# Kernel tuning notes

Measured on AMD Instinct MI355X. Metric: run time of the kernel, lower is better.

Reference implementation:

```python
import jax, jax.numpy as jnp
import numpy as np

B, S, T = 32, 256, 256
V, E, H, C, SE = 10000, 512, 1024, 1024, 8


def _gru_cell(x, h, Wih, Whh, bih, bhh):
    # torch.nn.GRUCell math; Wih: [3H, in], Whh: [3H, H]
    gi = x @ Wih.T + bih
    gh = h @ Whh.T + bhh
    ir, iz, inn = jnp.split(gi, 3, axis=-1)
    hr, hz, hn = jnp.split(gh, 3, axis=-1)
    r = jax.nn.sigmoid(ir + hr)
    z = jax.nn.sigmoid(iz + hz)
    n = jnp.tanh(inn + r * hn)
    return (1.0 - z) * n + z * h


def setup_inputs() -> dict:
    key = jax.random.key(0)
    ks = jax.random.split(key, 20)
    s = 0.02
    emb_table = jax.random.normal(ks[0], (V, E), jnp.float32) * s
    emb_table = emb_table.at[0].set(0.0)  # padding_idx = 0
    style_table = jax.random.normal(ks[1], (2, SE), jnp.float32)
    in1 = E + SE + C
    inp = {
        "enc_output": jax.random.normal(ks[2], (B, S, C), jnp.float32),
        "enc_len": jax.random.randint(ks[3], (B,), 1, S + 1),
        "styles": jax.random.randint(ks[4], (B,), 0, 2),
        "dec_in": jax.random.randint(ks[5], (B, T), 0, V),
        "dec_out": jax.random.randint(ks[6], (B, T), 0, V),
        "emb_table": emb_table,
        "style_table": style_table,
        "Wp": jax.random.normal(ks[7], (H, C + SE), jnp.float32) * s,
        "bp": jnp.zeros((H,), jnp.float32),
        "Wih1": jax.random.normal(ks[8], (3 * H, in1), jnp.float32) * s,
        "Whh1": jax.random.normal(ks[9], (3 * H, H), jnp.float32) * s,
        "bih1": jnp.zeros((3 * H,), jnp.float32),
        "bhh1": jnp.zeros((3 * H,), jnp.float32),
        "Wih2": jax.random.normal(ks[10], (3 * H, H), jnp.float32) * s,
        "Whh2": jax.random.normal(ks[11], (3 * H, H), jnp.float32) * s,
        "bih2": jnp.zeros((3 * H,), jnp.float32),
        "bhh2": jnp.zeros((3 * H,), jnp.float32),
        "Wout": jax.random.normal(ks[12], (H, V), jnp.float32) * s,
        "bout": jnp.zeros((V,), jnp.float32),
    }
    return inp


def reference(enc_output, enc_len, styles, dec_in, dec_out, emb_table, style_table,
              Wp, bp, Wih1, Whh1, bih1, bhh1, Wih2, Whh2, bih2, bhh2, Wout, bout):
    batch = enc_output.shape[0]
    # get_enc_context: encoder output at last valid timestep
    last = jnp.clip(enc_len - 1, 0, enc_output.shape[1] - 1)
    ctx = enc_output[jnp.arange(batch), last]              # [B, C]
    style_emb = style_table[styles]                         # [B, SE]
    # init hidden state: project(concat(ctx, style_emb))
    h0 = jnp.concatenate([ctx, style_emb], -1) @ Wp.T + bp  # [B, H]
    h1 = jnp.zeros_like(h0)
    # constant part of cell input (no attention: context fixed)
    sc = jnp.concatenate([style_emb, ctx], -1)              # [B, SE+C]
    emb_seq = emb_table[dec_in].transpose(1, 0, 2)          # [T, B, E]

    def step(carry, emb_t):
        a, b = carry
        x = jnp.concatenate([emb_t, sc], -1)
        a = _gru_cell(x, a, Wih1, Whh1, bih1, bhh1)
        b = _gru_cell(a, b, Wih2, Whh2, bih2, bhh2)
        return (a, b), b

    _, h1s = jax.lax.scan(step, (h0, h1), emb_seq)          # [T, B, H]
    logits = jnp.einsum('tbh,hv->btv', h1s, Wout) + bout    # [B, T, V]
    log_probs = jax.nn.log_softmax(logits, axis=2)
    prediction = jnp.argmax(logits, axis=-1)                # [B, T]
    dec_output_log_probs = jnp.take_along_axis(log_probs, dec_out[..., None], axis=2)[..., 0]
    return logits, dec_output_log_probs, prediction
```

## Files before the change

### kernel.cpp

```cpp
#include <hip/hip_runtime.h>
#include <math.h>

#define NBLK 256
#define GROUPS 16
#define GSIZE 16

__device__ __forceinline__ float sigf(float x) { return 1.0f / (1.0f + __expf(-x)); }

__global__ void prep_kernel(const float* __restrict__ enc_output,
                            const int*   __restrict__ enc_len,
                            const int*   __restrict__ styles,
                            const float* __restrict__ style_table,
                            float* __restrict__ xA,
                            float* __restrict__ xB,
                            float* __restrict__ bT0)
{
    int b = blockIdx.x;
    int tid = threadIdx.x;
    int last = enc_len[b] - 1;
    last = last < 0 ? 0 : (last > 255 ? 255 : last);
    const float* ctx = enc_output + ((size_t)b * 256 + last) * 1024;
    for (int k = tid; k < 1024; k += blockDim.x) {
        float v = ctx[k];
        xA[b * 1032 + k]     = v;
        xB[b * 1032 + 8 + k] = v;
        bT0[b * 1024 + k]    = 0.0f;
    }
    if (tid < 8) {
        float se = style_table[styles[b] * 8 + tid];
        xA[b * 1032 + 1024 + tid] = se;
        xB[b * 1032 + tid]        = se;
    }
}

template<int BMODE, int EPI, int GATHER>
__global__ __launch_bounds__(256, 2)
void gemm128(const float* __restrict__ A, int lda,
             const float* __restrict__ W, int ldb,
             const float* __restrict__ bias,
             const float* __restrict__ rowbase,
             const int*   __restrict__ gidx,
             float* __restrict__ Cout,
             int M, int N, int K)
{
    __shared__ float As[8][132];
    __shared__ float Bs[8][132];
    const int tid = threadIdx.x;
    const int r0 = blockIdx.x * 128;
    const int n0 = blockIdx.y * 128;
    const int tx = tid & 15;
    const int ty = tid >> 4;

    float acc[8][8];
#pragma unroll
    for (int i = 0; i < 8; ++i)
#pragma unroll
        for (int j = 0; j < 8; ++j) acc[i][j] = 0.0f;

    const int am  = tid >> 1;
    const int akq = (tid & 1) * 4;
    const bool avalid = (r0 + am) < M;
    const float* arow;
    {
        int r = r0 + am; if (r >= M) r = M - 1;
        if (GATHER) {
            int idx = gidx[(r & 31) * 256 + (r >> 5)];
            arow = A + (size_t)idx * lda;
        } else {
            arow = A + (size_t)r * lda;
        }
    }

    for (int k0 = 0; k0 < K; k0 += 8) {
        float4 av = make_float4(0.f, 0.f, 0.f, 0.f);
        if (avalid) av = *(const float4*)(arow + k0 + akq);

        if (BMODE == 0) {
            const int ncol = tid >> 1;
            const int kq   = (tid & 1) * 4;
            float4 bv = make_float4(0.f, 0.f, 0.f, 0.f);
            int j = n0 + ncol;
            if (j < N) bv = *(const float4*)(W + (size_t)j * ldb + k0 + kq);
            __syncthreads();
            As[akq + 0][am] = av.x; As[akq + 1][am] = av.y;
            As[akq + 2][am] = av.z; As[akq + 3][am] = av.w;
            Bs[kq + 0][ncol] = bv.x; Bs[kq + 1][ncol] = bv.y;
            Bs[kq + 2][ncol] = bv.z; Bs[kq + 3][ncol] = bv.w;
        } else {
            const int kk = tid >> 5;
            const int nq = (tid & 31) * 4;
            float4 bv = make_float4(0.f, 0.f, 0.f, 0.f);
            int j = n0 + nq;
            if (j < N) bv = *(const float4*)(W + (size_t)(k0 + kk) * ldb + j);
            __syncthreads();
            As[akq + 0][am] = av.x; As[akq + 1][am] = av.y;
            As[akq + 2][am] = av.z; As[akq + 3][am] = av.w;
            *(float4*)&Bs[kk][nq] = bv;
        }
        __syncthreads();

#pragma unroll
        for (int kk = 0; kk < 8; ++kk) {
            float4 a0 = *(const float4*)&As[kk][ty * 8];
            float4 a1 = *(const float4*)&As[kk][ty * 8 + 4];
            float4 b0 = *(const float4*)&Bs[kk][tx * 8];
            float4 b1 = *(const float4*)&Bs[kk][tx * 8 + 4];
            float ar[8] = {a0.x, a0.y, a0.z, a0.w, a1.x, a1.y, a1.z, a1.w};
            float br[8] = {b0.x, b0.y, b0.z, b0.w, b1.x, b1.y, b1.z, b1.w};
#pragma unroll
            for (int i = 0; i < 8; ++i)
#pragma unroll
                for (int j = 0; j < 8; ++j)
                    acc[i][j] = fmaf(ar[i], br[j], acc[i][j]);
        }
    }

#pragma unroll
    for (int i = 0; i < 8; ++i) {
        int r = r0 + ty * 8 + i;
        if (r >= M) continue;
        const float* rb = rowbase ? (rowbase + (size_t)(r & 31) * N) : nullptr;
#pragma unroll
        for (int jq = 0; jq < 2; ++jq) {
            int n = n0 + tx * 8 + jq * 4;
            if (n >= N) continue;
            float4 v;
            v.x = acc[i][jq * 4 + 0]; v.y = acc[i][jq * 4 + 1];
            v.z = acc[i][jq * 4 + 2]; v.w = acc[i][jq * 4 + 3];
            if (bias) {
                float4 bz = *(const float4*)(bias + n);
                v.x += bz.x; v.y += bz.y; v.z += bz.z; v.w += bz.w;
            }
            if (rb) {
                float4 rz = *(const float4*)(rb + n);
                v.x += rz.x; v.y += rz.y; v.z += rz.z; v.w += rz.w;
            }
            if (EPI == 2) {
                size_t basei = (size_t)(r >> 5) * (size_t)N * 32 + (size_t)(r & 31);
                Cout[basei + (size_t)(n + 0) * 32] = v.x;
                Cout[basei + (size_t)(n + 1) * 32] = v.y;
                Cout[basei + (size_t)(n + 2) * 32] = v.z;
                Cout[basei + (size_t)(n + 3) * 32] = v.w;
            } else if (EPI == 3) {
                *(float4*)(Cout + (size_t)(n >> 2) * 128 + (size_t)(r & 31) * 4) = v;
            } else {
                float* crow = (EPI == 0) ? (Cout + (size_t)r * N)
                                         : (Cout + (size_t)((r & 31) * 256 + (r >> 5)) * (size_t)N);
                *(float4*)(crow + n) = v;
            }
        }
    }
}

__device__ __forceinline__ float4 coh_load4(const float4* p) {
    const unsigned long long* q = (const unsigned long long*)p;
    union { float4 f; unsigned long long u[2]; } cv;
    cv.u[0] = __hip_atomic_load((unsigned long long*)q,     __ATOMIC_RELAXED, __HIP_MEMORY_SCOPE_AGENT);
    cv.u[1] = __hip_atomic_load((unsigned long long*)q + 1, __ATOMIC_RELAXED, __HIP_MEMORY_SCOPE_AGENT);
    return cv.f;
}
__device__ __forceinline__ void coh_store4(float4* p, float4 v) {
    unsigned long long* q = (unsigned long long*)p;
    union { float4 f; unsigned long long u[2]; } cv; cv.f = v;
    __hip_atomic_store(q,     cv.u[0], __ATOMIC_RELAXED, __HIP_MEMORY_SCOPE_AGENT);
    __hip_atomic_store(q + 1, cv.u[1], __ATOMIC_RELAXED, __HIP_MEMORY_SCOPE_AGENT);
}

__device__ __forceinline__ void grid_sync(int* bar, int epoch, int grp) {
    __syncthreads();
    if (threadIdx.x == 0) {
        int prev = __hip_atomic_fetch_add(bar + grp * 64, 1, __ATOMIC_RELAXED, __HIP_MEMORY_SCOPE_AGENT);
        if (prev == epoch * GSIZE - 1) {
            int rprev = __hip_atomic_fetch_add(bar + 1024, 1, __ATOMIC_RELAXED, __HIP_MEMORY_SCOPE_AGENT);
            if (rprev == epoch * GROUPS - 1) {
#pragma unroll
                for (int j = 0; j < GROUPS; ++j)
                    __hip_atomic_store(bar + 1088 + j * 64, epoch, __ATOMIC_RELAXED, __HIP_MEMORY_SCOPE_AGENT);
            }
        }
        int spins = 0;
        while (__hip_atomic_load(bar + 1088 + grp * 64, __ATOMIC_RELAXED, __HIP_MEMORY_SCOPE_AGENT) < epoch) {
            __builtin_amdgcn_s_sleep(8);
            if (++spins > (1 << 20)) break;
        }
    }
    __syncthreads();
}

__global__ __launch_bounds__(512, 2)
void scan_persistent(const float* __restrict__ gi1T,
                     float* __restrict__ aT,
                     float* __restrict__ bT,
                     float* __restrict__ bSeq,
                     float* __restrict__ gbuf,
                     const float* __restrict__ Whh1, const float* __restrict__ bhh1,
                     const float* __restrict__ Wih2, const float* __restrict__ bih2,
                     const float* __restrict__ Whh2, const float* __restrict__ bhh2,
                     int* __restrict__ barP)
{
    __shared__ float wlds[36864];
    __shared__ float part[8][9][32];
    __shared__ float gsum[9][32];

    const int tid = threadIdx.x;
    const int b   = tid & 31;
    const int kk  = (tid >> 5) & 1;
    const int ks  = tid >> 6;
    const int bk  = blockIdx.x;
    const int grp = bk >> 4;
    const int koff = ks * 128 + kk * 64;
    const int role = tid >> 5;

    for (int c = tid; c < 9216; c += 512) {
        int k4 = c & 255;
        int uv = c >> 8;
        int ul = uv / 9, v = uv - ul * 9;
        int u  = bk * 4 + ul;
        const float* W = (v < 3) ? Whh1 : (v < 6 ? Wih2 : Whh2);
        int g = v % 3;
        float4 w = *(const float4*)(W + ((size_t)(g * 1024 + u)) * 1024 + k4 * 4);
        *(float4*)&wlds[(size_t)uv * 1024 + k4 * 4] = w;
    }

    float wb[3][4];
    if (tid < 96) {
        const float* bias = (role == 0) ? bhh1 : (role == 1 ? bih2 : bhh2);
#pragma unroll
        for (int g = 0; g < 3; ++g)
#pragma unroll
            for (int ul = 0; ul < 4; ++ul)
                wb[g][ul] = bias[g * 1024 + bk * 4 + ul];
    }
    __syncthreads();

    float aOut[4] = {0, 0, 0, 0};
    float bOut[4] = {0, 0, 0, 0};

    for (int s = 0; s <= 257; ++s) {
        const bool doL1 = (s <= 255);
        const bool doG2 = (s >= 1 && s <= 256);
        const bool doL2 = (s >= 2);
        const bool doA  = doL1 || doG2;
        const int slot  = s & 1;

        float pgi[3][4];
        float4 hprev = make_float4(0.f, 0.f, 0.f, 0.f);
        if (role == 0 && doL1) {
            const float* gi = gi1T + (size_t)s * 98304;
#pragma unroll
            for (int g = 0; g < 3; ++g)
#pragma unroll
                for (int ul = 0; ul < 4; ++ul)
                    pgi[g][ul] = gi[(g * 1024 + bk * 4 + ul) * 32 + b];
            hprev = coh_load4((const float4*)aT + (size_t)slot * 8192 + bk * 32 + b);
        } else if (role == 2 && doL2) {
            const float* g2 = gbuf + (size_t)((s + 1) & 1) * 98304;
#pragma unroll
            for (int g = 0; g < 3; ++g)
#pragma unroll
                for (int ul = 0; ul < 4; ++ul)
                    pgi[g][ul] = g2[(g * 1024 + bk * 4 + ul) * 32 + b];
            hprev = coh_load4((const float4*)bT + (size_t)slot * 8192 + bk * 32 + b);
        }

        float accA[6][4], accC[3][4];
#pragma unroll
        for (int v = 0; v < 6; ++v)
#pragma unroll
            for (int ul = 0; ul < 4; ++ul) accA[v][ul] = 0.f;
#pragma unroll
        for (int v = 0; v < 3; ++v)
#pragma unroll
            for (int ul = 0; ul < 4; ++ul) accC[v][ul] = 0.f;

        if (doA) {
            float4 hA[16];
            const float4* src = (const float4*)aT + (size_t)slot * 8192 + b;
#pragma unroll
            for (int i = 0; i < 16; ++i) hA[i] = coh_load4(src + (size_t)((ks * 32 + kk * 16 + i) * 32));
#pragma unroll
            for (int ul = 0; ul < 4; ++ul)
#pragma unroll
                for (int v = 0; v < 6; ++v) {
                    const float4* w = (const float4*)&wlds[(ul * 9 + v) * 1024 + koff];
                    float s0 = 0.f, s1 = 0.f, s2 = 0.f, s3 = 0.f;
#pragma unroll
                    for (int i = 0; i < 16; ++i) {
                        float4 wv = w[i];
                        s0 = fmaf(hA[i].x, wv.x, s0);
                        s1 = fmaf(hA[i].y, wv.y, s1);
                        s2 = fmaf(hA[i].z, wv.z, s2);
                        s3 = fmaf(hA[i].w, wv.w, s3);
                    }
                    accA[v][ul] = (s0 + s1) + (s2 + s3);
                }
        }
        if (doL2) {
            float4 hB[16];
            const float4* src = (const float4*)bT + (size_t)slot * 8192 + b;
#pragma unroll
            for (int i = 0; i < 16; ++i) hB[i] = coh_load4(src + (size_t)((ks * 32 + kk * 16 + i) * 32));
#pragma unroll
            for (int ul = 0; ul < 4; ++ul)
#pragma unroll
                for (int v = 0; v < 3; ++v) {
                    const float4* w = (const float4*)&wlds[(ul * 9 + 6 + v) * 1024 + koff];
                    float s0 = 0.f, s1 = 0.f, s2 = 0.f, s3 = 0.f;
#pragma unroll
                    for (int i = 0; i < 16; ++i) {
                        float4 wv = w[i];
                        s0 = fmaf(hB[i].x, wv.x, s0);
                        s1 = fmaf(hB[i].y, wv.y, s1);
                        s2 = fmaf(hB[i].z, wv.z, s2);
                        s3 = fmaf(hB[i].w, wv.w, s3);
                    }
                    accC[v][ul] = (s0 + s1) + (s2 + s3);
                }
        }

#pragma unroll
        for (int v = 0; v < 6; ++v)
#pragma unroll
            for (int ul = 0; ul < 4; ++ul)
                accA[v][ul] += __shfl_xor(accA[v][ul], 32);
#pragma unroll
        for (int v = 0; v < 3; ++v)
#pragma unroll
            for (int ul = 0; ul < 4; ++ul)
                accC[v][ul] += __shfl_xor(accC[v][ul], 32);

#pragma unroll
        for (int ul = 0; ul < 4; ++ul) {
            if (kk == 0) {
#pragma unroll
                for (int v = 0; v < 6; ++v) part[ks][v][b] = accA[v][ul];
#pragma unroll
                for (int v = 0; v < 3; ++v) part[ks][6 + v][b] = accC[v][ul];
            }
            __syncthreads();
            if (tid < 288) {
                int v = tid >> 5, bb = tid & 31;
                float s8 = 0.f;
#pragma unroll
                for (int r = 0; r < 8; ++r) s8 += part[r][v][bb];
                gsum[v][bb] = s8;
            }
            __syncthreads();
            if (tid < 96) {
                const int u = bk * 4 + ul;
                if (role == 0) {
                    if (doL1) {
                        float r = sigf(pgi[0][ul] + gsum[0][b] + wb[0][ul]);
                        float z = sigf(pgi[1][ul] + gsum[1][b] + wb[1][ul]);
                        float n = tanhf(pgi[2][ul] + r * (gsum[2][b] + wb[2][ul]));
                        float hp = (ul == 0) ? hprev.x : (ul == 1) ? hprev.y : (ul == 2) ? hprev.z : hprev.w;
                        aOut[ul] = (1.0f - z) * n + z * hp;
                    }
                } else if (role == 1) {
                    if (doG2) {
                        float* g2 = gbuf + (size_t)(s & 1) * 98304;
#pragma unroll
                        for (int g = 0; g < 3; ++g)
                            g2[(g * 1024 + u) * 32 + b] = gsum[3 + g][b] + wb[g][ul];
                    }
                } else {
                    if (doL2) {
                        float r = sigf(pgi[0][ul] + gsum[6][b] + wb[0][ul]);
                        float z = sigf(pgi[1][ul] + gsum[7][b] + wb[1][ul]);
                        float n = tanhf(pgi[2][ul] + r * (gsum[8][b] + wb[2][ul]));
                        float hp = (ul == 0) ? hprev.x : (ul == 1) ? hprev.y : (ul == 2) ? hprev.z : hprev.w;
                        bOut[ul] = (1.0f - z) * n + z * hp;
                    }
                }
            }
        }

        if (role == 0 && doL1) {
            float4 o = make_float4(aOut[0], aOut[1], aOut[2], aOut[3]);
            coh_store4((float4*)aT + (size_t)((s + 1) & 1) * 8192 + bk * 32 + b, o);
        }
        if (role == 2 && doL2) {
            float4 o = make_float4(bOut[0], bOut[1], bOut[2], bOut[3]);
            coh_store4((float4*)bT + (size_t)((s + 1) & 1) * 8192 + bk * 32 + b, o);
            *(float4*)(bSeq + (size_t)(s - 1) * 32768 + (size_t)b * 1024 + bk * 4) = o;
        }

        grid_sync(barP, s + 1, grp);
    }
}

__global__ __launch_bounds__(256)
void softmax_tail(const float* __restrict__ logits,
                  const int*   __restrict__ dec_out,
                  float* __restrict__ lp,
                  float* __restrict__ pred)
{
    const int p = blockIdx.x;
    const int tid = threadIdx.x;
    const float* row = logits + (size_t)p * 10000;

    float m = -INFINITY, s = 0.0f;
    int am = 0;
    for (int q = tid; q < 2500; q += 256) {
        float4 v = *(const float4*)(row + q * 4);
        float xs[4] = {v.x, v.y, v.z, v.w};
#pragma unroll
        for (int c = 0; c < 4; ++c) {
            float x = xs[c];
            if (x > m) {
                s = s * __expf(m - x) + 1.0f;
                m = x;
                am = q * 4 + c;
            } else {
                s += __expf(x - m);
            }
        }
    }
    __shared__ float sm[256];
    __shared__ float ss[256];
    __shared__ int   sa[256];
    sm[tid] = m; ss[tid] = s; sa[tid] = am;
    __syncthreads();
    for (int w = 128; w > 0; w >>= 1) {
        if (tid < w) {
            float m1 = sm[tid],     s1 = ss[tid];     int a1 = sa[tid];
            float m2 = sm[tid + w], s2 = ss[tid + w]; int a2 = sa[tid + w];
            float M2 = fmaxf(m1, m2);
            float S2 = s1 * __expf(m1 - M2) + s2 * __expf(m2 - M2);
            int A2;
            if (m1 > m2) A2 = a1;
            else if (m2 > m1) A2 = a2;
            else A2 = (a1 < a2) ? a1 : a2;
            sm[tid] = M2; ss[tid] = S2; sa[tid] = A2;
        }
        __syncthreads();
    }
    if (tid == 0) {
        float lse = sm[0] + logf(ss[0]);
        int tok = dec_out[p];
        lp[p]   = row[tok] - lse;
        pred[p] = (float)sa[0];
    }
}

extern "C" void kernel_launch(void* const* d_in, const int* in_sizes, int n_in,
                              void* d_out, int out_size, void* d_ws, size_t ws_size,
                              hipStream_t stream)
{
    const float* enc_output  = (const float*)d_in[0];
    const int*   enc_len     = (const int*)  d_in[1];
    const int*   styles      = (const int*)  d_in[2];
    const int*   dec_in      = (const int*)  d_in[3];
    const int*   dec_out     = (const int*)  d_in[4];
    const float* emb_table   = (const float*)d_in[5];
    const float* style_table = (const float*)d_in[6];
    const float* Wp   = (const float*)d_in[7];
    const float* bp   = (const float*)d_in[8];
    const float* Wih1 = (const float*)d_in[9];
    const float* Whh1 = (const float*)d_in[10];
    const float* bih1 = (const float*)d_in[11];
    const float* bhh1 = (const float*)d_in[12];
    const float* Wih2 = (const float*)d_in[13];
    const float* Whh2 = (const float*)d_in[14];
    const float* bih2 = (const float*)d_in[15];
    const float* bhh2 = (const float*)d_in[16];
    const float* Wout = (const float*)d_in[17];
    const float* bout = (const float*)d_in[18];

    float* out = (float*)d_out;

    float* gi1T  = out;
    float* aT    = out + 25165824;
    float* bTr   = out + 25231360;
    float* base1 = out + 25296896;
    float* xA    = out + 25395200;
    float* xB    = out + 25428224;
    float* gbuf  = out + 25461248;
    int*   barP  = (int*)(out + 25657856);
    float* bSeq  = (float*)d_ws;

    float* logitsOut = out;
    float* lpOut     = out + 81920000;
    float* predOut   = out + 81928192;

    prep_kernel<<<32, 256, 0, stream>>>(enc_output, enc_len, styles, style_table, xA, xB, bTr);

    gemm128<0, 3, 0><<<dim3(1, 8), 256, 0, stream>>>(xA, 1032, Wp, 1032, bp, nullptr, nullptr,
                                                     aT, 32, 1024, 1032);
    gemm128<0, 0, 0><<<dim3(1, 24), 256, 0, stream>>>(xB, 1032, Wih1 + 512, 1544, bih1, nullptr, nullptr,
                                                      base1, 32, 3072, 1032);
    gemm128<0, 2, 1><<<dim3(64, 24), 256, 0, stream>>>(emb_table, 512, Wih1, 1544, nullptr, base1, dec_in,
                                                       gi1T, 8192, 3072, 512);

    hipMemsetAsync(barP, 0, 8448, stream);

    scan_persistent<<<NBLK, 512, 0, stream>>>(gi1T, aT, bTr, bSeq, gbuf,
                                              Whh1, bhh1, Wih2, bih2, Whh2, bhh2,
                                              barP);

    gemm128<1, 1, 0><<<dim3(64, 79), 256, 0, stream>>>(bSeq + 32768, 1024, Wout, 10000, bout, nullptr, nullptr,
                                                       logitsOut, 8192, 10000, 1024);
    softmax_tail<<<8192, 256, 0, stream>>>(logitsOut, dec_out, lpOut, predOut);
}
```

Before: 9.293 ms.

## Register-block two batches per thread in persistent GRU scan with swizzled LDS weights

Reworks the thread mapping in the persistent scan so each lane handles two batch columns over a narrower k-slice. Each LDS weight load is then reused for two FMAs chains, and the weight layout is swizzled per 8-float4 group to avoid bank conflicts when 4 k-subgroups read together. Hidden-state loads for both layers are hoisted to the top of the step so they can issue early. The reduction gains an extra shuffle stage, register pressure grows from holding 32 float4 hidden values, and the barrier spin sleep is shortened.

```diff
diff --git a/kernel.cpp b/kernel.cpp
--- a/kernel.cpp
+++ b/kernel.cpp
@@ -152,18 +152,18 @@
     }
 }
 
+__device__ __forceinline__ void coh_store4(float4* p, float4 v) {
+    unsigned long long* q = (unsigned long long*)p;
+    union { float4 f; unsigned long long u[2]; } cv; cv.f = v;
+    __hip_atomic_store(q,     cv.u[0], __ATOMIC_RELAXED, __HIP_MEMORY_SCOPE_AGENT);
+    __hip_atomic_store(q + 1, cv.u[1], __ATOMIC_RELAXED, __HIP_MEMORY_SCOPE_AGENT);
+}
 __device__ __forceinline__ float4 coh_load4(const float4* p) {
     const unsigned long long* q = (const unsigned long long*)p;
     union { float4 f; unsigned long long u[2]; } cv;
     cv.u[0] = __hip_atomic_load((unsigned long long*)q,     __ATOMIC_RELAXED, __HIP_MEMORY_SCOPE_AGENT);
     cv.u[1] = __hip_atomic_load((unsigned long long*)q + 1, __ATOMIC_RELAXED, __HIP_MEMORY_SCOPE_AGENT);
     return cv.f;
-}
-__device__ __forceinline__ void coh_store4(float4* p, float4 v) {
-    unsigned long long* q = (unsigned long long*)p;
-    union { float4 f; unsigned long long u[2]; } cv; cv.f = v;
-    __hip_atomic_store(q,     cv.u[0], __ATOMIC_RELAXED, __HIP_MEMORY_SCOPE_AGENT);
-    __hip_atomic_store(q + 1, cv.u[1], __ATOMIC_RELAXED, __HIP_MEMORY_SCOPE_AGENT);
 }
 
 __device__ __forceinline__ void grid_sync(int* bar, int epoch, int grp) {
@@ -180,7 +180,7 @@
         }
         int spins = 0;
         while (__hip_atomic_load(bar + 1088 + grp * 64, __ATOMIC_RELAXED, __HIP_MEMORY_SCOPE_AGENT) < epoch) {
-            __builtin_amdgcn_s_sleep(8);
+            __builtin_amdgcn_s_sleep(2);
             if (++spins > (1 << 20)) break;
         }
     }
@@ -202,24 +202,30 @@
     __shared__ float part[8][9][32];
     __shared__ float gsum[9][32];
 
-    const int tid = threadIdx.x;
-    const int b   = tid & 31;
-    const int kk  = (tid >> 5) & 1;
-    const int ks  = tid >> 6;
-    const int bk  = blockIdx.x;
-    const int grp = bk >> 4;
-    const int koff = ks * 128 + kk * 64;
+    const int tid  = threadIdx.x;
+    const int lane = tid & 63;
+    const int bq   = lane & 15;
+    const int ksub = lane >> 4;
+    const int ks   = tid >> 6;
+    const int bk   = blockIdx.x;
+    const int grp  = bk >> 4;
+    const int b0   = bq * 2, b1 = b0 + 1;
+    const int kq0  = ks * 32 + ksub * 8;
     const int role = tid >> 5;
+    const int bw   = tid & 31;
+
+    float4* wlds4 = (float4*)wlds;
 
     for (int c = tid; c < 9216; c += 512) {
-        int k4 = c & 255;
+        int kq = c & 255;
         int uv = c >> 8;
         int ul = uv / 9, v = uv - ul * 9;
         int u  = bk * 4 + ul;
         const float* W = (v < 3) ? Whh1 : (v < 6 ? Wih2 : Whh2);
         int g = v % 3;
-        float4 w = *(const float4*)(W + ((size_t)(g * 1024 + u)) * 1024 + k4 * 4);
-        *(float4*)&wlds[(size_t)uv * 1024 + k4 * 4] = w;
+        float4 w = *(const float4*)(W + ((size_t)(g * 1024 + u)) * 1024 + kq * 4);
+        int pos = uv * 256 + (kq & ~7) + ((kq + ((kq >> 3) & 3)) & 7);
+        wlds4[pos] = w;
     }
 
     float wb[3][4];
@@ -243,6 +249,26 @@
         const bool doA  = doL1 || doG2;
         const int slot  = s & 1;
 
+        float4 hA0[8], hA1[8], hB0[8], hB1[8];
+        if (doA) {
+            const float4* srcA = (const float4*)aT + (size_t)slot * 8192;
+#pragma unroll
+            for (int o = 0; o < 8; ++o) {
+                int kq = kq0 + ((o + 8 - ksub) & 7);
+                hA0[o] = coh_load4(srcA + (size_t)kq * 32 + b0);
+                hA1[o] = coh_load4(srcA + (size_t)kq * 32 + b1);
+            }
+        }
+        if (doL2) {
+            const float4* srcB = (const float4*)bT + (size_t)slot * 8192;
+#pragma unroll
+            for (int o = 0; o < 8; ++o) {
+                int kq = kq0 + ((o + 8 - ksub) & 7);
+                hB0[o] = coh_load4(srcB + (size_t)kq * 32 + b0);
+                hB1[o] = coh_load4(srcB + (size_t)kq * 32 + b1);
+            }
+        }
+
         float pgi[3][4];
         float4 hprev = make_float4(0.f, 0.f, 0.f, 0.f);
         if (role == 0 && doL1) {
@@ -251,91 +277,91 @@
             for (int g = 0; g < 3; ++g)
 #pragma unroll
                 for (int ul = 0; ul < 4; ++ul)
-                    pgi[g][ul] = gi[(g * 1024 + bk * 4 + ul) * 32 + b];
-            hprev = coh_load4((const float4*)aT + (size_t)slot * 8192 + bk * 32 + b);
+                    pgi[g][ul] = gi[(g * 1024 + bk * 4 + ul) * 32 + bw];
+            hprev = coh_load4((const float4*)aT + (size_t)slot * 8192 + bk * 32 + bw);
         } else if (role == 2 && doL2) {
             const float* g2 = gbuf + (size_t)((s + 1) & 1) * 98304;
 #pragma unroll
             for (int g = 0; g < 3; ++g)
 #pragma unroll
                 for (int ul = 0; ul < 4; ++ul)
-                    pgi[g][ul] = g2[(g * 1024 + bk * 4 + ul) * 32 + b];
-            hprev = coh_load4((const float4*)bT + (size_t)slot * 8192 + bk * 32 + b);
-        }
-
-        float accA[6][4], accC[3][4];
-#pragma unroll
-        for (int v = 0; v < 6; ++v)
-#pragma unroll
-            for (int ul = 0; ul < 4; ++ul) accA[v][ul] = 0.f;
-#pragma unroll
-        for (int v = 0; v < 3; ++v)
-#pragma unroll
-            for (int ul = 0; ul < 4; ++ul) accC[v][ul] = 0.f;
+                    pgi[g][ul] = g2[(g * 1024 + bk * 4 + ul) * 32 + bw];
+            hprev = coh_load4((const float4*)bT + (size_t)slot * 8192 + bk * 32 + bw);
+        }
+
+        float accA[4][6][2];
+        float accC[4][3][2];
+#pragma unroll
+        for (int ul = 0; ul < 4; ++ul) {
+#pragma unroll
+            for (int v = 0; v < 6; ++v) { accA[ul][v][0] = 0.f; accA[ul][v][1] = 0.f; }
+#pragma unroll
+            for (int v = 0; v < 3; ++v) { accC[ul][v][0] = 0.f; accC[ul][v][1] = 0.f; }
+        }
 
         if (doA) {
-            float4 hA[16];
-            const float4* src = (const float4*)aT + (size_t)slot * 8192 + b;
-#pragma unroll
-            for (int i = 0; i < 16; ++i) hA[i] = coh_load4(src + (size_t)((ks * 32 + kk * 16 + i) * 32));
 #pragma unroll
             for (int ul = 0; ul < 4; ++ul)
 #pragma unroll
                 for (int v = 0; v < 6; ++v) {
-                    const float4* w = (const float4*)&wlds[(ul * 9 + v) * 1024 + koff];
-                    float s0 = 0.f, s1 = 0.f, s2 = 0.f, s3 = 0.f;
-#pragma unroll
-                    for (int i = 0; i < 16; ++i) {
-                        float4 wv = w[i];
-                        s0 = fmaf(hA[i].x, wv.x, s0);
-                        s1 = fmaf(hA[i].y, wv.y, s1);
-                        s2 = fmaf(hA[i].z, wv.z, s2);
-                        s3 = fmaf(hA[i].w, wv.w, s3);
+                    const float4* wp = wlds4 + (ul * 9 + v) * 256 + kq0;
+                    float s0 = 0.f, s1 = 0.f;
+#pragma unroll
+                    for (int o = 0; o < 8; ++o) {
+                        float4 w = wp[o];
+                        s0 = fmaf(hA0[o].x, w.x, fmaf(hA0[o].y, w.y, fmaf(hA0[o].z, w.z, fmaf(hA0[o].w, w.w, s0))));
+                        s1 = fmaf(hA1[o].x, w.x, fmaf(hA1[o].y, w.y, fmaf(hA1[o].z, w.z, fmaf(hA1[o].w, w.w, s1))));
                     }
-                    accA[v][ul] = (s0 + s1) + (s2 + s3);
+                    accA[ul][v][0] = s0; accA[ul][v][1] = s1;
                 }
         }
         if (doL2) {
-            float4 hB[16];
-            const float4* src = (const float4*)bT + (size_t)slot * 8192 + b;
-#pragma unroll
-            for (int i = 0; i < 16; ++i) hB[i] = coh_load4(src + (size_t)((ks * 32 + kk * 16 + i) * 32));
 #pragma unroll
             for (int ul = 0; ul < 4; ++ul)
 #pragma unroll
                 for (int v = 0; v < 3; ++v) {
-                    const float4* w = (const float4*)&wlds[(ul * 9 + 6 + v) * 1024 + koff];
-                    float s0 = 0.f, s1 = 0.f, s2 = 0.f, s3 = 0.f;
-#pragma unroll
-                    for (int i = 0; i < 16; ++i) {
-                        float4 wv = w[i];
-                        s0 = fmaf(hB[i].x, wv.x, s0);
-                        s1 = fmaf(hB[i].y, wv.y, s1);
-                        s2 = fmaf(hB[i].z, wv.z, s2);
-                        s3 = fmaf(hB[i].w, wv.w, s3);
+                    const float4* wp = wlds4 + (ul * 9 + 6 + v) * 256 + kq0;
+                    float s0 = 0.f, s1 = 0.f;
+#pragma unroll
+                    for (int o = 0; o < 8; ++o) {
+                        float4 w = wp[o];
+                        s0 = fmaf(hB0[o].x, w.x, fmaf(hB0[o].y, w.y, fmaf(hB0[o].z, w.z, fmaf(hB0[o].w, w.w, s0))));
+                        s1 = fmaf(hB1[o].x, w.x, fmaf(hB1[o].y, w.y, fmaf(hB1[o].z, w.z, fmaf(hB1[o].w, w.w, s1))));
                     }
-                    accC[v][ul] = (s0 + s1) + (s2 + s3);
-                }
-        }
-
-#pragma unroll
-        for (int v = 0; v < 6; ++v)
-#pragma unroll
-            for (int ul = 0; ul < 4; ++ul)
-                accA[v][ul] += __shfl_xor(accA[v][ul], 32);
-#pragma unroll
-        for (int v = 0; v < 3; ++v)
-#pragma unroll
-            for (int ul = 0; ul < 4; ++ul)
-                accC[v][ul] += __shfl_xor(accC[v][ul], 32);
+                    accC[ul][v][0] = s0; accC[ul][v][1] = s1;
+                }
+        }
+
+#pragma unroll
+        for (int d = 16; d <= 32; d <<= 1) {
+#pragma unroll
+            for (int ul = 0; ul < 4; ++ul) {
+#pragma unroll
+                for (int v = 0; v < 6; ++v) {
+                    accA[ul][v][0] += __shfl_xor(accA[ul][v][0], d);
+                    accA[ul][v][1] += __shfl_xor(accA[ul][v][1], d);
+                }
+#pragma unroll
+                for (int v = 0; v < 3; ++v) {
+                    accC[ul][v][0] += __shfl_xor(accC[ul][v][0], d);
+                    accC[ul][v][1] += __shfl_xor(accC[ul][v][1], d);
+                }
+            }
+        }
 
 #pragma unroll
         for (int ul = 0; ul < 4; ++ul) {
-            if (kk == 0) {
-#pragma unroll
-                for (int v = 0; v < 6; ++v) part[ks][v][b] = accA[v][ul];
-#pragma unroll
-                for (int v = 0; v < 3; ++v) part[ks][6 + v][b] = accC[v][ul];
+            if (ksub == 0) {
+#pragma unroll
+                for (int v = 0; v < 6; ++v) {
+                    part[ks][v][b0] = accA[ul][v][0];
+                    part[ks][v][b1] = accA[ul][v][1];
+                }
+#pragma unroll
+                for (int v = 0; v < 3; ++v) {
+                    part[ks][6 + v][b0] = accC[ul][v][0];
+                    part[ks][6 + v][b1] = accC[ul][v][1];
+                }
             }
             __syncthreads();
             if (tid < 288) {
@@ -350,9 +376,9 @@
                 const int u = bk * 4 + ul;
                 if (role == 0) {
                     if (doL1) {
-                        float r = sigf(pgi[0][ul] + gsum[0][b] + wb[0][ul]);
-                        float z = sigf(pgi[1][ul] + gsum[1][b] + wb[1][ul]);
-                        float n = tanhf(pgi[2][ul] + r * (gsum[2][b] + wb[2][ul]));
+                        float r = sigf(pgi[0][ul] + gsum[0][bw] + wb[0][ul]);
+                        float z = sigf(pgi[1][ul] + gsum[1][bw] + wb[1][ul]);
+                        float n = tanhf(pgi[2][ul] + r * (gsum[2][bw] + wb[2][ul]));
                         float hp = (ul == 0) ? hprev.x : (ul == 1) ? hprev.y : (ul == 2) ? hprev.z : hprev.w;
                         aOut[ul] = (1.0f - z) * n + z * hp;
                     }
@@ -361,13 +387,13 @@
                         float* g2 = gbuf + (size_t)(s & 1) * 98304;
 #pragma unroll
                         for (int g = 0; g < 3; ++g)
-                            g2[(g * 1024 + u) * 32 + b] = gsum[3 + g][b] + wb[g][ul];
+                            g2[(g * 1024 + u) * 32 + bw] = gsum[3 + g][bw] + wb[g][ul];
                     }
                 } else {
                     if (doL2) {
-                        float r = sigf(pgi[0][ul] + gsum[6][b] + wb[0][ul]);
-                        float z = sigf(pgi[1][ul] + gsum[7][b] + wb[1][ul]);
-                        float n = tanhf(pgi[2][ul] + r * (gsum[8][b] + wb[2][ul]));
+                        float r = sigf(pgi[0][ul] + gsum[6][bw] + wb[0][ul]);
+                        float z = sigf(pgi[1][ul] + gsum[7][bw] + wb[1][ul]);
+                        float n = tanhf(pgi[2][ul] + r * (gsum[8][bw] + wb[2][ul]));
                         float hp = (ul == 0) ? hprev.x : (ul == 1) ? hprev.y : (ul == 2) ? hprev.z : hprev.w;
                         bOut[ul] = (1.0f - z) * n + z * hp;
                     }
@@ -377,12 +403,12 @@
 
         if (role == 0 && doL1) {
             float4 o = make_float4(aOut[0], aOut[1], aOut[2], aOut[3]);
-            coh_store4((float4*)aT + (size_t)((s + 1) & 1) * 8192 + bk * 32 + b, o);
+            coh_store4((float4*)aT + (size_t)((s + 1) & 1) * 8192 + bk * 32 + bw, o);
         }
         if (role == 2 && doL2) {
             float4 o = make_float4(bOut[0], bOut[1], bOut[2], bOut[3]);
-            coh_store4((float4*)bT + (size_t)((s + 1) & 1) * 8192 + bk * 32 + b, o);
-            *(float4*)(bSeq + (size_t)(s - 1) * 32768 + (size_t)b * 1024 + bk * 4) = o;
+            coh_store4((float4*)bT + (size_t)((s + 1) & 1) * 8192 + bk * 32 + bw, o);
+            *(float4*)(bSeq + (size_t)(s - 1) * 32768 + (size_t)bw * 1024 + bk * 4) = o;
         }
 
         grid_sync(barP, s + 1, grp);
```

Result: slower. 14.75 ms (+58.7%).
